# Performance work log

Hardware: AMD Instinct MI355X
Metric: run time of the kernel (lower is better)

The kernel has to match this reference:

```python
import jax, jax.numpy as jnp
import numpy as np

N = 100000   # nodes
E = 300000   # directed edges
NG = 4096    # graphs in batch
F_IN = 22
HID = 128


def setup_inputs() -> dict:
    key = jax.random.key(0)
    ks = jax.random.split(key, 32)
    s = 0.05
    inp = {
        "x": jax.random.normal(ks[0], (N, F_IN), jnp.float32),
        "edge_index": jax.random.randint(ks[1], (2, E), 0, N),
        "batch": jnp.sort(jax.random.randint(ks[2], (N,), 0, NG)),
        # GAT layer 1: 22 -> 4 heads x 32
        "W1": jax.random.normal(ks[3], (F_IN, HID), jnp.float32) * s,
        "as1": jax.random.normal(ks[4], (4, 32), jnp.float32) * s,
        "ad1": jax.random.normal(ks[5], (4, 32), jnp.float32) * s,
        "b1": jnp.zeros((HID,), jnp.float32),
        "g1": jnp.ones((HID,), jnp.float32),
        "be1": jnp.zeros((HID,), jnp.float32),
        # GAT layer 2: 128 -> 4 heads x 32
        "W2": jax.random.normal(ks[6], (HID, HID), jnp.float32) * s,
        "as2": jax.random.normal(ks[7], (4, 32), jnp.float32) * s,
        "ad2": jax.random.normal(ks[8], (4, 32), jnp.float32) * s,
        "b2": jnp.zeros((HID,), jnp.float32),
        "g2": jnp.ones((HID,), jnp.float32),
        "be2": jnp.zeros((HID,), jnp.float32),
        # GAT layer 3: 128 -> 1 head x 128
        "W3": jax.random.normal(ks[9], (HID, HID), jnp.float32) * s,
        "as3": jax.random.normal(ks[10], (1, HID), jnp.float32) * s,
        "ad3": jax.random.normal(ks[11], (1, HID), jnp.float32) * s,
        "b3": jnp.zeros((HID,), jnp.float32),
        "g3": jnp.ones((HID,), jnp.float32),
        "be3": jnp.zeros((HID,), jnp.float32),
        # MLP head
        "fw1": jax.random.normal(ks[12], (HID, 64), jnp.float32) * s,
        "fb1": jnp.zeros((64,), jnp.float32),
        "fw2": jax.random.normal(ks[13], (64, 1), jnp.float32) * s,
        "fb2": jnp.zeros((1,), jnp.float32),
    }
    return inp


def reference(x, edge_index, batch, W1, as1, ad1, b1, g1, be1,
              W2, as2, ad2, b2, g2, be2, W3, as3, ad3, b3, g3, be3,
              fw1, fb1, fw2, fb2):
    n = x.shape[0]
    sl = jnp.arange(n)
    src = jnp.concatenate([edge_index[0], sl])  # PyG GATConv adds self-loops
    dst = jnp.concatenate([edge_index[1], sl])

    def gat(h_in, W, a_s, a_d, b):
        H, C = a_s.shape
        h = (h_in @ W).reshape(n, H, C)                      # [N,H,C]
        al_s = jnp.einsum('nhc,hc->nh', h, a_s)              # per-node src score
        al_d = jnp.einsum('nhc,hc->nh', h, a_d)
        e = jax.nn.leaky_relu(al_s[src] + al_d[dst], 0.2)    # [Etot,H]
        emax = jax.ops.segment_max(e, dst, num_segments=n)
        ex = jnp.exp(e - emax[dst])
        den = jax.ops.segment_sum(ex, dst, num_segments=n)
        alpha = ex / (den[dst] + 1e-16)                       # segment softmax over in-edges
        msg = h[src] * alpha[:, :, None]                      # [Etot,H,C]
        out = jax.ops.segment_sum(msg, dst, num_segments=n)
        return out.reshape(n, H * C) + b

    def bn(h, g, be):
        m = h.mean(0)
        v = h.var(0)
        return (h - m) * jax.lax.rsqrt(v + 1e-5) * g + be

    h = jax.nn.relu(bn(gat(x, W1, as1, ad1, b1), g1, be1))
    h = jax.nn.relu(bn(gat(h, W2, as2, ad2, b2), g2, be2))
    h = jax.nn.relu(bn(gat(h, W3, as3, ad3, b3), g3, be3))

    # global mean pool over graphs
    s = jax.ops.segment_sum(h, batch, num_segments=NG)
    cnt = jax.ops.segment_sum(jnp.ones((n,), h.dtype), batch, num_segments=NG)
    pooled = s / jnp.maximum(cnt, 1.0)[:, None]

    z = jax.nn.relu(pooled @ fw1 + fb1)
    return z @ fw2 + fb2
```

## Files before the change

### kernel.cpp

```cpp
#include <hip/hip_runtime.h>

#define N_NODES 100000
#define N_EDGES 300000
#define N_ETOT  400000
#define NGRAPH  4096
#define HID     128
#define NBLK_SCAN 391
#define PNPB    32
#define STATS_BLOCKS 512
#define NSLICE  64

typedef __attribute__((ext_vector_type(8))) short short8;
typedef __attribute__((ext_vector_type(8))) ushort ushort8;
typedef __attribute__((ext_vector_type(4))) float f32x4;

__device__ __forceinline__ ushort f2bf(float f) {
    union { float f; unsigned u; } x; x.f = f;
    unsigned r = x.u + 0x7FFF + ((x.u >> 16) & 1);
    return (ushort)(r >> 16);
}

__device__ __forceinline__ float bf2f(ushort v) {
    union { unsigned u; float f; } t;
    t.u = ((unsigned)v) << 16;
    return t.f;
}

__device__ __forceinline__ float2 bf2f2(unsigned v) {
    union { unsigned u; float f; } lo, hi;
    lo.u = v << 16;
    hi.u = v & 0xFFFF0000u;
    return make_float2(lo.f, hi.f);
}

#define SETUP_W      36864
#define SETUP_SUMS   (SETUP_W + NSLICE * 256)
#define SETUP_CNTS   (SETUP_SUMS + N_NODES)
#define SETUP_TOT    (SETUP_CNTS + NGRAPH * HID + NGRAPH)
__global__ __launch_bounds__(256) void setup_kernel(
    const float* __restrict__ W1, const float* __restrict__ W2, const float* __restrict__ W3,
    ushort* __restrict__ Wt1, ushort* __restrict__ Wt2, ushort* __restrict__ Wt3,
    float* __restrict__ sums_sl, int* __restrict__ counts,
    float* __restrict__ pooled)
{
    const int i = blockIdx.x * 256 + threadIdx.x;
    if (i < 16384) {
        int c = i >> 7, k = i & 127;
        Wt2[c * 128 + k] = f2bf(W2[k * 128 + c]);
    } else if (i < 32768) {
        int j = i - 16384; int c = j >> 7, k = j & 127;
        Wt3[c * 128 + k] = f2bf(W3[k * 128 + c]);
    } else if (i < SETUP_W) {
        int j = i - 32768; int c = j >> 5, k = j & 31;
        Wt1[c * 32 + k] = (k < 22) ? f2bf(W1[k * 128 + c]) : (ushort)0;
    } else if (i < SETUP_SUMS) {
        sums_sl[i - SETUP_W] = 0.f;
    } else if (i < SETUP_CNTS) {
        counts[i - SETUP_SUMS] = 0;
    } else if (i < SETUP_TOT) {
        pooled[i - SETUP_CNTS] = 0.f;
    }
}

template<int K, bool PRE_BN, int HH, bool DX>
__global__ __launch_bounds__(256) void mfma_gemm_kernel(
    const ushort* __restrict__ Ab, const float* __restrict__ Af,
    const ushort* __restrict__ Wt,
    const float* __restrict__ scale, const float* __restrict__ shift,
    const float* __restrict__ avs, const float* __restrict__ avd,
    ushort* __restrict__ Cb, float* __restrict__ als, float* __restrict__ ald, int M)
{
    constexpr int SEGS = K / 8;
    constexpr int SSH  = (K == 128) ? 4 : 2;
    constexpr int SWM  = SEGS - 1;
    constexpr int NP   = SEGS / 2;
    constexpr int KT   = K / 32;

    __shared__ ushort Asm[128 * K];
    __shared__ ushort Bsm[128 * K];

    const int tid  = threadIdx.x;
    const int wave = tid >> 6;
    const int lane = tid & 63;
    const int ln   = lane & 15;
    const int quad = lane >> 4;
    const int wr0  = (wave >> 1) * 64;
    const int wc0  = (wave & 1) * 64;
    const int row0 = blockIdx.x * 128;

    short8 aR[NP], wR[NP];
    #pragma unroll
    for (int q = 0; q < NP; ++q) {
        const int chunk = tid + q * 256;
        const int r   = chunk >> SSH;
        const int seg = chunk & SWM;
        if constexpr (DX) {
            const int rr = min(row0 + r, N_NODES - 1);
            #pragma unroll
            for (int i = 0; i < 8; ++i) {
                const int c = seg * 8 + i;
                const float f = (c < 22) ? Af[(size_t)rr * 22 + c] : 0.f;
                aR[q][i] = (short)f2bf(f);
            }
        } else {
            aR[q] = *(const short8*)&Ab[(size_t)(row0 + r) * K + seg * 8];
        }
        wR[q] = *(const short8*)&Wt[(size_t)r * K + seg * 8];
    }
    if constexpr (PRE_BN) {
        #pragma unroll
        for (int q = 0; q < NP; ++q) {
            const int seg = (tid + q * 256) & SWM;
            const int cc  = seg * 8;
            #pragma unroll
            for (int i = 0; i < 8; ++i) {
                float f = bf2f((ushort)aR[q][i]);
                f = fmaxf(f * scale[cc + i] + shift[cc + i], 0.f);
                aR[q][i] = (short)f2bf(f);
            }
        }
    }
    #pragma unroll
    for (int q = 0; q < NP; ++q) {
        const int chunk = tid + q * 256;
        const int r   = chunk >> SSH;
        const int seg = chunk & SWM;
        const int sp  = seg ^ (r & SWM);
        *(short8*)&Asm[r * K + sp * 8] = aR[q];
        *(short8*)&Bsm[r * K + sp * 8] = wR[q];
    }
    __syncthreads();

    f32x4 acc[4][4] = {};
    #pragma unroll
    for (int kt = 0; kt < KT; ++kt) {
        short8 af[4], bf[4];
        #pragma unroll
        for (int i = 0; i < 4; ++i) {
            const int ra = wr0 + i * 16 + ln;
            const int ca = wc0 + i * 16 + ln;
            af[i] = *(const short8*)&Asm[ra * K + (((kt * 4 + quad) ^ (ra & SWM)) * 8)];
            bf[i] = *(const short8*)&Bsm[ca * K + (((kt * 4 + quad) ^ (ca & SWM)) * 8)];
        }
        #pragma unroll
        for (int tr = 0; tr < 4; ++tr)
            #pragma unroll
            for (int tc = 0; tc < 4; ++tc)
                acc[tr][tc] = __builtin_amdgcn_mfma_f32_16x16x32_bf16(
                    af[tr], bf[tc], acc[tr][tc], 0, 0, 0);
    }

    #pragma unroll
    for (int tr = 0; tr < 4; ++tr)
        #pragma unroll
        for (int rg = 0; rg < 4; ++rg) {
            const int gr = row0 + wr0 + tr * 16 + quad * 4 + rg;
            if (gr < M) {
                #pragma unroll
                for (int tc = 0; tc < 4; ++tc)
                    Cb[(size_t)gr * HID + wc0 + tc * 16 + ln] = f2bf(acc[tr][tc][rg]);
            }
        }

    __syncthreads();
    float* ps = (float*)Asm;
    float* pd = (float*)Bsm;
    #pragma unroll
    for (int tr = 0; tr < 4; ++tr)
      #pragma unroll
      for (int rg = 0; rg < 4; ++rg) {
        float sA = 0.f, sB = 0.f, dA = 0.f, dB = 0.f;
        #pragma unroll
        for (int tc = 0; tc < 4; ++tc) {
            const int col = wc0 + tc * 16 + ln;
            const float v = acc[tr][tc][rg];
            if (tc < 2) { sA += v * avs[col]; dA += v * avd[col]; }
            else        { sB += v * avs[col]; dB += v * avd[col]; }
        }
        #pragma unroll
        for (int m = 1; m < 16; m <<= 1) {
            sA += __shfl_xor(sA, m); sB += __shfl_xor(sB, m);
            dA += __shfl_xor(dA, m); dB += __shfl_xor(dB, m);
        }
        if (ln == 0) {
            const int rl = wr0 + tr * 16 + quad * 4 + rg;
            const int h0 = (wave & 1) * 2;
            ps[rl * 4 + h0] = sA; ps[rl * 4 + h0 + 1] = sB;
            pd[rl * 4 + h0] = dA; pd[rl * 4 + h0 + 1] = dB;
        }
      }
    __syncthreads();
    {
        const int r  = tid & 127;
        const int gr = row0 + r;
        if (gr < M) {
            if (tid < 128) {
                if (HH == 4) {
                    #pragma unroll
                    for (int h = 0; h < 4; ++h) als[gr * 4 + h] = ps[r * 4 + h];
                } else als[gr] = ps[r * 4] + ps[r * 4 + 1] + ps[r * 4 + 2] + ps[r * 4 + 3];
            } else {
                if (HH == 4) {
                    #pragma unroll
                    for (int h = 0; h < 4; ++h) ald[gr * 4 + h] = pd[r * 4 + h];
                } else ald[gr] = pd[r * 4] + pd[r * 4 + 1] + pd[r * 4 + 2] + pd[r * 4 + 3];
            }
        }
    }
}

__global__ void hist_kernel(const int* __restrict__ ei, int* __restrict__ counts) {
    int e = blockIdx.x * blockDim.x + threadIdx.x;
    if (e >= N_ETOT) return;
    int dst = (e < N_EDGES) ? ei[N_EDGES + e] : e - N_EDGES;
    atomicAdd(&counts[dst], 1);
}

__global__ __launch_bounds__(256) void scanA_kernel(
    const int* __restrict__ counts, int* __restrict__ rowptr, int* __restrict__ bsum)
{
    __shared__ int ls[256];
    const int t = threadIdx.x;
    const int i = blockIdx.x * 256 + t;
    const int v = (i < N_NODES) ? counts[i] : 0;
    ls[t] = v; __syncthreads();
    #pragma unroll
    for (int off = 1; off < 256; off <<= 1) {
        int add = (t >= off) ? ls[t - off] : 0;
        __syncthreads();
        ls[t] += add;
        __syncthreads();
    }
    if (i < N_NODES) rowptr[i] = ls[t] - v;
    if (t == 255) bsum[blockIdx.x] = ls[255];
}

__global__ __launch_bounds__(256) void scanC_kernel(
    int* __restrict__ rowptr, const int* __restrict__ bsum, int* __restrict__ cursor)
{
    __shared__ int red[256];
    const int t = threadIdx.x;
    int s = 0;
    for (int b = t; b < (int)blockIdx.x; b += 256) s += bsum[b];
    red[t] = s;
    __syncthreads();
    #pragma unroll
    for (int off = 128; off; off >>= 1) {
        if (t < off) red[t] += red[t + off];
        __syncthreads();
    }
    const int base = red[0];
    const int i = blockIdx.x * 256 + t;
    if (i < N_NODES) {
        const int v = rowptr[i] + base;
        rowptr[i] = v;
        cursor[i] = v;
    }
    if (i == 0) rowptr[N_NODES] = N_ETOT;
}

__global__ void scatter_kernel(const int* __restrict__ ei, int* __restrict__ cursor,
                               int* __restrict__ psrc)
{
    int e = blockIdx.x * blockDim.x + threadIdx.x;
    if (e >= N_ETOT) return;
    int src, dst;
    if (e < N_EDGES) { src = ei[e]; dst = ei[N_EDGES + e]; }
    else             { src = dst = e - N_EDGES; }
    int pos = atomicAdd(&cursor[dst], 1);
    psrc[pos] = src;
}

template<int HH>
__global__ __launch_bounds__(256) void agg_kernel(
    const ushort* __restrict__ H, const float* __restrict__ als,
    const float* __restrict__ ald, const int* __restrict__ rowptr,
    const int* __restrict__ psrc, ushort* __restrict__ Outb)
{
    const int tid  = threadIdx.x;
    const int node = blockIdx.x * 4 + (tid >> 6);
    const int lane = tid & 63;
    const int grp  = lane >> 4;
    const int cl   = lane & 15;
    const int hd   = (HH == 4) ? (cl >> 2) : 0;
    const int r0 = rowptr[node];
    const int r1 = rowptr[node + 1];
    const float aldh = (HH == 4) ? ald[node * 4 + hd] : ald[node];

    float den = 0.f;
    float acc[8] = {};
    for (int p = r0 + grp; p < r1; p += 4) {
        const int src = psrc[p];
        float v = ((HH == 4) ? als[src * 4 + hd] : als[src]) + aldh;
        v = (v > 0.f) ? v : 0.2f * v;
        const float ex = __expf(v);
        const uint4 hv = *(const uint4*)&H[(size_t)src * HID + cl * 8];
        const float2 h0 = bf2f2(hv.x), h1 = bf2f2(hv.y);
        const float2 h2 = bf2f2(hv.z), h3 = bf2f2(hv.w);
        acc[0] += ex * h0.x; acc[1] += ex * h0.y;
        acc[2] += ex * h1.x; acc[3] += ex * h1.y;
        acc[4] += ex * h2.x; acc[5] += ex * h2.y;
        acc[6] += ex * h3.x; acc[7] += ex * h3.y;
        den += ex;
    }
    #pragma unroll
    for (int m = 16; m < 64; m <<= 1) {
        den += __shfl_xor(den, m);
        #pragma unroll
        for (int i = 0; i < 8; ++i) acc[i] += __shfl_xor(acc[i], m);
    }
    if (grp == 0) {
        const float inv = 1.f / (den + 1e-16f);
        ushort8 o;
        #pragma unroll
        for (int i = 0; i < 8; ++i) o[i] = f2bf(acc[i] * inv);
        *(ushort8*)&Outb[(size_t)node * HID + cl * 8] = o;
    }
}

__global__ __launch_bounds__(256) void bn_stats_kernel(
    const ushort* __restrict__ X, float* __restrict__ sums_sl)
{
    __shared__ float ls[16][128], lq[16][128];
    const int tid = threadIdx.x;
    const int ro  = tid >> 4;
    const int ci  = tid & 15;
    const int c0  = ci * 8;
    const int rpb = (N_NODES + STATS_BLOCKS - 1) / STATS_BLOCKS;
    const int r0  = blockIdx.x * rpb;
    const int r1  = min(r0 + rpb, N_NODES);

    float s[8] = {}, q[8] = {};
    for (int r = r0 + ro; r < r1; r += 16) {
        const ushort8 v = *(const ushort8*)&X[(size_t)r * HID + c0];
        #pragma unroll
        for (int j = 0; j < 8; ++j) {
            const float f = bf2f(v[j]);
            s[j] += f; q[j] += f * f;
        }
    }
    #pragma unroll
    for (int j = 0; j < 8; ++j) { ls[ro][c0 + j] = s[j]; lq[ro][c0 + j] = q[j]; }
    __syncthreads();
    const int half = tid >> 7;
    const int c    = tid & 127;
    float acc = 0.f;
    if (half == 0) {
        #pragma unroll
        for (int k = 0; k < 16; ++k) acc += ls[k][c];
    } else {
        #pragma unroll
        for (int k = 0; k < 16; ++k) acc += lq[k][c];
    }
    atomicAdd(&sums_sl[(blockIdx.x & (NSLICE - 1)) * 256 + tid], acc);
}

__global__ __launch_bounds__(256) void bn_finalize_kernel(
    float* __restrict__ sums_sl,
    const float* __restrict__ g, const float* __restrict__ be,
    float* __restrict__ scale, float* __restrict__ shift)
{
    __shared__ float red[256];
    const int tid = threadIdx.x;
    float s = 0.f;
    for (int b = 0; b < NSLICE; ++b) {
        s += sums_sl[b * 256 + tid];
        sums_sl[b * 256 + tid] = 0.f;
    }
    red[tid] = s;
    __syncthreads();
    if (tid < 128) {
        const float m = red[tid] * (1.f / N_NODES);
        const float v = red[tid + 128] * (1.f / N_NODES) - m * m;
        const float sc = g[tid] * rsqrtf(v + 1e-5f);
        scale[tid] = sc;
        shift[tid] = be[tid] - m * sc;
    }
}

__global__ __launch_bounds__(128) void bn_pool_kernel(
    const ushort* __restrict__ X, const float* __restrict__ scale, const float* __restrict__ shift,
    const int* __restrict__ batch, float* __restrict__ pooled, float* __restrict__ cnt)
{
    const int c = threadIdx.x;
    const int n0 = blockIdx.x * PNPB;
    const int n1 = min(n0 + PNPB, N_NODES);
    const float sc = scale[c], sh = shift[c];
    int gcur = batch[n0];
    float acc = 0.f;
    int run = 0;
    for (int n = n0; n < n1; ++n) {
        const int g = batch[n];
        if (g != gcur) {
            atomicAdd(&pooled[(size_t)gcur * HID + c], acc);
            if (c == 0) atomicAdd(&cnt[gcur], (float)run);
            acc = 0.f; run = 0; gcur = g;
        }
        const float v = bf2f(X[(size_t)n * HID + c]) * sc + sh;
        acc += fmaxf(v, 0.f);
        ++run;
    }
    atomicAdd(&pooled[(size_t)gcur * HID + c], acc);
    if (c == 0) atomicAdd(&cnt[gcur], (float)run);
}

__global__ __launch_bounds__(256) void mlp_kernel(
    const float* __restrict__ pooled, const float* __restrict__ cnt,
    const float* __restrict__ fw1, const float* __restrict__ fb1,
    const float* __restrict__ fw2, const float* __restrict__ fb2,
    float* __restrict__ out)
{
    __shared__ float w1[HID * 64];
    __shared__ float rows[4][HID];
    const int tid = threadIdx.x;
    for (int i = tid; i < HID * 64; i += 256) w1[i] = fw1[i];
    const int gl = tid >> 6;
    const int j  = tid & 63;
    const float b1 = fb1[j];
    const float w2 = fw2[j];
    __syncthreads();
    #pragma unroll
    for (int it = 0; it < 4; ++it) {
        const int g = blockIdx.x * 16 + it * 4 + gl;
        const float inv = 1.f / fmaxf(cnt[g], 1.f);
        rows[gl][j]      = pooled[(size_t)g * HID + j] * inv;
        rows[gl][j + 64] = pooled[(size_t)g * HID + 64 + j] * inv;
        __syncthreads();
        float z = b1;
        #pragma unroll 8
        for (int c2 = 0; c2 < HID; ++c2) z += rows[gl][c2] * w1[c2 * 64 + j];
        z = fmaxf(z, 0.f);
        float p = z * w2;
        #pragma unroll
        for (int off = 32; off; off >>= 1) p += __shfl_down(p, off);
        if (j == 0) out[g] = p + fb2[0];
        __syncthreads();
    }
}

extern "C" void kernel_launch(void* const* d_in, const int* in_sizes, int n_in,
                              void* d_out, int out_size, void* d_ws, size_t ws_size,
                              hipStream_t stream)
{
    const float* x     = (const float*)d_in[0];
    const int*   ei    = (const int*)d_in[1];
    const int*   batch = (const int*)d_in[2];
    const float* W1  = (const float*)d_in[3];
    const float* as1 = (const float*)d_in[4];
    const float* ad1 = (const float*)d_in[5];
    const float* g1  = (const float*)d_in[7];
    const float* be1 = (const float*)d_in[8];
    const float* W2  = (const float*)d_in[9];
    const float* as2 = (const float*)d_in[10];
    const float* ad2 = (const float*)d_in[11];
    const float* g2  = (const float*)d_in[13];
    const float* be2 = (const float*)d_in[14];
    const float* W3  = (const float*)d_in[15];
    const float* as3 = (const float*)d_in[16];
    const float* ad3 = (const float*)d_in[17];
    const float* g3  = (const float*)d_in[19];
    const float* be3 = (const float*)d_in[20];
    const float* fw1 = (const float*)d_in[21];
    const float* fb1 = (const float*)d_in[22];
    const float* fw2 = (const float*)d_in[23];
    const float* fb2 = (const float*)d_in[24];
    float* out = (float*)d_out;

    ushort* Hb  = (ushort*)d_ws;
    ushort* Bh  = Hb  + (size_t)N_NODES * HID;
    ushort* Wt1 = Bh  + (size_t)N_NODES * HID + 128 * 128;
    ushort* Wt2 = Wt1 + 128 * 32;
    ushort* Wt3 = Wt2 + 128 * 128;
    float* als    = (float*)(Wt3 + 128 * 128);
    float* ald    = als + (size_t)N_NODES * 4;
    float* sums_sl= ald + (size_t)N_NODES * 4;
    float* scale  = sums_sl + NSLICE * 256;
    float* shift  = scale + HID;
    float* pooled = shift + HID;
    float* cnt    = pooled + (size_t)NGRAPH * HID;
    int*   rowptr = (int*)(cnt + NGRAPH);
    int*   counts = rowptr + (N_NODES + 1);
    int*   cursor = counts + N_NODES;
    int*   bsum   = cursor + N_NODES;
    int*   psrc   = bsum + 512;

    auto cdiv = [](int a, int b) { return (a + b - 1) / b; };

    setup_kernel<<<cdiv(SETUP_TOT, 256), 256, 0, stream>>>(
        W1, W2, W3, Wt1, Wt2, Wt3, sums_sl, counts, pooled);

    hist_kernel<<<cdiv(N_ETOT, 256), 256, 0, stream>>>(ei, counts);
    scanA_kernel<<<NBLK_SCAN, 256, 0, stream>>>(counts, rowptr, bsum);
    scanC_kernel<<<NBLK_SCAN, 256, 0, stream>>>(rowptr, bsum, cursor);
    scatter_kernel<<<cdiv(N_ETOT, 256), 256, 0, stream>>>(ei, cursor, psrc);

    const int ggrid = cdiv(N_NODES, 128);
    const int agrid = N_NODES / 4;

    mfma_gemm_kernel<32, false, 4, true><<<ggrid, 256, 0, stream>>>(
        nullptr, x, Wt1, nullptr, nullptr, as1, ad1, Hb, als, ald, N_NODES);
    agg_kernel<4><<<agrid, 256, 0, stream>>>(Hb, als, ald, rowptr, psrc, Bh);
    bn_stats_kernel<<<STATS_BLOCKS, 256, 0, stream>>>(Bh, sums_sl);
    bn_finalize_kernel<<<1, 256, 0, stream>>>(sums_sl, g1, be1, scale, shift);

    mfma_gemm_kernel<128, true, 4, false><<<ggrid, 256, 0, stream>>>(
        Bh, nullptr, Wt2, scale, shift, as2, ad2, Hb, als, ald, N_NODES);
    agg_kernel<4><<<agrid, 256, 0, stream>>>(Hb, als, ald, rowptr, psrc, Bh);
    bn_stats_kernel<<<STATS_BLOCKS, 256, 0, stream>>>(Bh, sums_sl);
    bn_finalize_kernel<<<1, 256, 0, stream>>>(sums_sl, g2, be2, scale, shift);

    mfma_gemm_kernel<128, true, 1, false><<<ggrid, 256, 0, stream>>>(
        Bh, nullptr, Wt3, scale, shift, as3, ad3, Hb, als, ald, N_NODES);
    agg_kernel<1><<<agrid, 256, 0, stream>>>(Hb, als, ald, rowptr, psrc, Bh);
    bn_stats_kernel<<<STATS_BLOCKS, 256, 0, stream>>>(Bh, sums_sl);
    bn_finalize_kernel<<<1, 256, 0, stream>>>(sums_sl, g3, be3, scale, shift);

    bn_pool_kernel<<<cdiv(N_NODES, PNPB), 128, 0, stream>>>(Bh, scale, shift, batch, pooled, cnt);
    mlp_kernel<<<NGRAPH / 16, 256, 0, stream>>>(pooled, cnt, fw1, fb1, fw2, fb2, out);
}
```

Before: 358.4 us.

## Fuse BN finalize into consumer kernels and read GEMM weights from global

Removes the three single-block bn_finalize launches. The GEMM and pool kernels now each reduce the slice sums and compute the BN scale and shift themselves. Per-layer sums buffers are used so no zeroing pass is needed, and the slice count drops from 64 to 8 to make the per-block reduction cheap, at the cost of more atomic contention in bn_stats. The GEMM also stops staging weights in LDS and loads the B fragments straight from global or L2, which halves LDS use but adds uncoalesced global reads inside the MFMA loop.

```diff
diff --git a/kernel.cpp b/kernel.cpp
--- a/kernel.cpp
+++ b/kernel.cpp
@@ -8,7 +8,7 @@
 #define NBLK_SCAN 391
 #define PNPB    32
 #define STATS_BLOCKS 512
-#define NSLICE  64
+#define NSLICE  8
 
 typedef __attribute__((ext_vector_type(8))) short short8;
 typedef __attribute__((ext_vector_type(8))) ushort ushort8;
@@ -34,13 +34,13 @@
 }
 
 #define SETUP_W      36864
-#define SETUP_SUMS   (SETUP_W + NSLICE * 256)
+#define SETUP_SUMS   (SETUP_W + 3 * NSLICE * 256)
 #define SETUP_CNTS   (SETUP_SUMS + N_NODES)
 #define SETUP_TOT    (SETUP_CNTS + NGRAPH * HID + NGRAPH)
 __global__ __launch_bounds__(256) void setup_kernel(
     const float* __restrict__ W1, const float* __restrict__ W2, const float* __restrict__ W3,
     ushort* __restrict__ Wt1, ushort* __restrict__ Wt2, ushort* __restrict__ Wt3,
-    float* __restrict__ sums_sl, int* __restrict__ counts,
+    float* __restrict__ sums_base, int* __restrict__ counts,
     float* __restrict__ pooled)
 {
     const int i = blockIdx.x * 256 + threadIdx.x;
@@ -54,7 +54,7 @@
         int j = i - 32768; int c = j >> 5, k = j & 31;
         Wt1[c * 32 + k] = (k < 22) ? f2bf(W1[k * 128 + c]) : (ushort)0;
     } else if (i < SETUP_SUMS) {
-        sums_sl[i - SETUP_W] = 0.f;
+        sums_base[i - SETUP_W] = 0.f;
     } else if (i < SETUP_CNTS) {
         counts[i - SETUP_SUMS] = 0;
     } else if (i < SETUP_TOT) {
@@ -66,7 +66,7 @@
 __global__ __launch_bounds__(256) void mfma_gemm_kernel(
     const ushort* __restrict__ Ab, const float* __restrict__ Af,
     const ushort* __restrict__ Wt,
-    const float* __restrict__ scale, const float* __restrict__ shift,
+    const float* __restrict__ sums, const float* __restrict__ g, const float* __restrict__ be,
     const float* __restrict__ avs, const float* __restrict__ avd,
     ushort* __restrict__ Cb, float* __restrict__ als, float* __restrict__ ald, int M)
 {
@@ -77,7 +77,7 @@
     constexpr int KT   = K / 32;
 
     __shared__ ushort Asm[128 * K];
-    __shared__ ushort Bsm[128 * K];
+    __shared__ float scsh[256];
 
     const int tid  = threadIdx.x;
     const int wave = tid >> 6;
@@ -88,7 +88,7 @@
     const int wc0  = (wave & 1) * 64;
     const int row0 = blockIdx.x * 128;
 
-    short8 aR[NP], wR[NP];
+    short8 aR[NP];
     #pragma unroll
     for (int q = 0; q < NP; ++q) {
         const int chunk = tid + q * 256;
@@ -105,9 +105,22 @@
         } else {
             aR[q] = *(const short8*)&Ab[(size_t)(row0 + r) * K + seg * 8];
         }
-        wR[q] = *(const short8*)&Wt[(size_t)r * K + seg * 8];
     }
     if constexpr (PRE_BN) {
+        if (tid < 128) {
+            float s = 0.f, q2 = 0.f;
+            #pragma unroll
+            for (int b = 0; b < NSLICE; ++b) {
+                s  += sums[b * 256 + tid];
+                q2 += sums[b * 256 + 128 + tid];
+            }
+            const float m  = s * (1.f / N_NODES);
+            const float v  = q2 * (1.f / N_NODES) - m * m;
+            const float sc = g[tid] * rsqrtf(v + 1e-5f);
+            scsh[tid]       = sc;
+            scsh[tid + 128] = be[tid] - m * sc;
+        }
+        __syncthreads();
         #pragma unroll
         for (int q = 0; q < NP; ++q) {
             const int seg = (tid + q * 256) & SWM;
@@ -115,7 +128,7 @@
             #pragma unroll
             for (int i = 0; i < 8; ++i) {
                 float f = bf2f((ushort)aR[q][i]);
-                f = fmaxf(f * scale[cc + i] + shift[cc + i], 0.f);
+                f = fmaxf(f * scsh[cc + i] + scsh[128 + cc + i], 0.f);
                 aR[q][i] = (short)f2bf(f);
             }
         }
@@ -127,7 +140,6 @@
         const int seg = chunk & SWM;
         const int sp  = seg ^ (r & SWM);
         *(short8*)&Asm[r * K + sp * 8] = aR[q];
-        *(short8*)&Bsm[r * K + sp * 8] = wR[q];
     }
     __syncthreads();
 
@@ -140,7 +152,7 @@
             const int ra = wr0 + i * 16 + ln;
             const int ca = wc0 + i * 16 + ln;
             af[i] = *(const short8*)&Asm[ra * K + (((kt * 4 + quad) ^ (ra & SWM)) * 8)];
-            bf[i] = *(const short8*)&Bsm[ca * K + (((kt * 4 + quad) ^ (ca & SWM)) * 8)];
+            bf[i] = *(const short8*)&Wt[(size_t)ca * K + (kt * 4 + quad) * 8];
         }
         #pragma unroll
         for (int tr = 0; tr < 4; ++tr)
@@ -164,7 +176,7 @@
 
     __syncthreads();
     float* ps = (float*)Asm;
-    float* pd = (float*)Bsm;
+    float* pd = (float*)(Asm + 1024);
     #pragma unroll
     for (int tr = 0; tr < 4; ++tr)
       #pragma unroll
@@ -355,46 +367,34 @@
     atomicAdd(&sums_sl[(blockIdx.x & (NSLICE - 1)) * 256 + tid], acc);
 }
 
-__global__ __launch_bounds__(256) void bn_finalize_kernel(
-    float* __restrict__ sums_sl,
-    const float* __restrict__ g, const float* __restrict__ be,
-    float* __restrict__ scale, float* __restrict__ shift)
-{
-    __shared__ float red[256];
-    const int tid = threadIdx.x;
-    float s = 0.f;
+__global__ __launch_bounds__(128) void bn_pool_kernel(
+    const ushort* __restrict__ X,
+    const float* __restrict__ sums, const float* __restrict__ g, const float* __restrict__ be,
+    const int* __restrict__ batch, float* __restrict__ pooled, float* __restrict__ cnt)
+{
+    const int c = threadIdx.x;
+    float s = 0.f, q2 = 0.f;
+    #pragma unroll
     for (int b = 0; b < NSLICE; ++b) {
-        s += sums_sl[b * 256 + tid];
-        sums_sl[b * 256 + tid] = 0.f;
-    }
-    red[tid] = s;
-    __syncthreads();
-    if (tid < 128) {
-        const float m = red[tid] * (1.f / N_NODES);
-        const float v = red[tid + 128] * (1.f / N_NODES) - m * m;
-        const float sc = g[tid] * rsqrtf(v + 1e-5f);
-        scale[tid] = sc;
-        shift[tid] = be[tid] - m * sc;
-    }
-}
-
-__global__ __launch_bounds__(128) void bn_pool_kernel(
-    const ushort* __restrict__ X, const float* __restrict__ scale, const float* __restrict__ shift,
-    const int* __restrict__ batch, float* __restrict__ pooled, float* __restrict__ cnt)
-{
-    const int c = threadIdx.x;
+        s  += sums[b * 256 + c];
+        q2 += sums[b * 256 + 128 + c];
+    }
+    const float m  = s * (1.f / N_NODES);
+    const float vv = q2 * (1.f / N_NODES) - m * m;
+    const float sc = g[c] * rsqrtf(vv + 1e-5f);
+    const float sh = be[c] - m * sc;
+
     const int n0 = blockIdx.x * PNPB;
     const int n1 = min(n0 + PNPB, N_NODES);
-    const float sc = scale[c], sh = shift[c];
     int gcur = batch[n0];
     float acc = 0.f;
     int run = 0;
     for (int n = n0; n < n1; ++n) {
-        const int g = batch[n];
-        if (g != gcur) {
+        const int gg = batch[n];
+        if (gg != gcur) {
             atomicAdd(&pooled[(size_t)gcur * HID + c], acc);
             if (c == 0) atomicAdd(&cnt[gcur], (float)run);
-            acc = 0.f; run = 0; gcur = g;
+            acc = 0.f; run = 0; gcur = gg;
         }
         const float v = bf2f(X[(size_t)n * HID + c]) * sc + sh;
         acc += fmaxf(v, 0.f);
@@ -473,10 +473,10 @@
     ushort* Wt3 = Wt2 + 128 * 128;
     float* als    = (float*)(Wt3 + 128 * 128);
     float* ald    = als + (size_t)N_NODES * 4;
-    float* sums_sl= ald + (size_t)N_NODES * 4;
-    float* scale  = sums_sl + NSLICE * 256;
-    float* shift  = scale + HID;
-    float* pooled = shift + HID;
+    float* sums1  = ald + (size_t)N_NODES * 4;
+    float* sums2  = sums1 + NSLICE * 256;
+    float* sums3  = sums2 + NSLICE * 256;
+    float* pooled = sums3 + NSLICE * 256;
     float* cnt    = pooled + (size_t)NGRAPH * HID;
     int*   rowptr = (int*)(cnt + NGRAPH);
     int*   counts = rowptr + (N_NODES + 1);
@@ -487,7 +487,7 @@
     auto cdiv = [](int a, int b) { return (a + b - 1) / b; };
 
     setup_kernel<<<cdiv(SETUP_TOT, 256), 256, 0, stream>>>(
-        W1, W2, W3, Wt1, Wt2, Wt3, sums_sl, counts, pooled);
+        W1, W2, W3, Wt1, Wt2, Wt3, sums1, counts, pooled);
 
     hist_kernel<<<cdiv(N_ETOT, 256), 256, 0, stream>>>(ei, counts);
     scanA_kernel<<<NBLK_SCAN, 256, 0, stream>>>(counts, rowptr, bsum);
@@ -498,23 +498,21 @@
     const int agrid = N_NODES / 4;
 
     mfma_gemm_kernel<32, false, 4, true><<<ggrid, 256, 0, stream>>>(
-        nullptr, x, Wt1, nullptr, nullptr, as1, ad1, Hb, als, ald, N_NODES);
+        nullptr, x, Wt1, nullptr, nullptr, nullptr, as1, ad1, Hb, als, ald, N_NODES);
     agg_kernel<4><<<agrid, 256, 0, stream>>>(Hb, als, ald, rowptr, psrc, Bh);
-    bn_stats_kernel<<<STATS_BLOCKS, 256, 0, stream>>>(Bh, sums_sl);
-    bn_finalize_kernel<<<1, 256, 0, stream>>>(sums_sl, g1, be1, scale, shift);
+    bn_stats_kernel<<<STATS_BLOCKS, 256, 0, stream>>>(Bh, sums1);
 
     mfma_gemm_kernel<128, true, 4, false><<<ggrid, 256, 0, stream>>>(
-        Bh, nullptr, Wt2, scale, shift, as2, ad2, Hb, als, ald, N_NODES);
+        Bh, nullptr, Wt2, sums1, g1, be1, as2, ad2, Hb, als, ald, N_NODES);
     agg_kernel<4><<<agrid, 256, 0, stream>>>(Hb, als, ald, rowptr, psrc, Bh);
-    bn_stats_kernel<<<STATS_BLOCKS, 256, 0, stream>>>(Bh, sums_sl);
-    bn_finalize_kernel<<<1, 256, 0, stream>>>(sums_sl, g2, be2, scale, shift);
+    bn_stats_kernel<<<STATS_BLOCKS, 256, 0, stream>>>(Bh, sums2);
 
     mfma_gemm_kernel<128, true, 1, false><<<ggrid, 256, 0, stream>>>(
-        Bh, nullptr, Wt3, scale, shift, as3, ad3, Hb, als, ald, N_NODES);
+        Bh, nullptr, Wt3, sums2, g2, be2, as3, ad3, Hb, als, ald, N_NODES);
     agg_kernel<1><<<agrid, 256, 0, stream>>>(Hb, als, ald, rowptr, psrc, Bh);
-    bn_stats_kernel<<<STATS_BLOCKS, 256, 0, stream>>>(Bh, sums_sl);
-    bn_finalize_kernel<<<1, 256, 0, stream>>>(sums_sl, g3, be3, scale, shift);
-
-    bn_pool_kernel<<<cdiv(N_NODES, PNPB), 128, 0, stream>>>(Bh, scale, shift, batch, pooled, cnt);
+    bn_stats_kernel<<<STATS_BLOCKS, 256, 0, stream>>>(Bh, sums3);
+
+    bn_pool_kernel<<<cdiv(N_NODES, PNPB), 128, 0, stream>>>(
+        Bh, sums3, g3, be3, batch, pooled, cnt);
     mlp_kernel<<<NGRAPH / 16, 256, 0, stream>>>(pooled, cnt, fw1, fb1, fw2, fb2, out);
 }
```

Measured after the change: 368.0 us. 2.7% more time.
